# Kernel tuning notes

Measured on AMD Instinct MI355X. Metric: run time of the kernel, lower is better.

Reference implementation:

```python
import math
import jax, jax.numpy as jnp
import numpy as np

SCALE = math.sqrt(128.0)  # NOTE: original code MULTIPLIES by sqrt(128)
DROPOUT_P = 0.1


def setup_inputs() -> dict:
    key = jax.random.key(0)
    kq, kk, kv = jax.random.split(key, 3)
    B, Q, V, H = 4, 4096, 4096, 128
    return {
        "query": jax.random.normal(kq, (B, Q, H), dtype=jnp.float32),
        "key": jax.random.normal(kk, (B, V, H), dtype=jnp.float32),
        "value": jax.random.normal(kv, (B, V, H), dtype=jnp.float32),
    }


def reference(query, key, value):
    # qk: [B, Q, V]
    qk = jnp.einsum("bqh,bvh->bqv", query, key)
    scaled_qk = qk * SCALE
    softmax_qk = jax.nn.softmax(scaled_qk, axis=-1)
    # inverted dropout with a fixed RNG key (deterministic reference)
    dk = jax.random.key(42)
    keep = jax.random.bernoulli(dk, 1.0 - DROPOUT_P, softmax_qk.shape)
    dropout_qk = jnp.where(keep, softmax_qk / (1.0 - DROPOUT_P), 0.0)
    # output: [B, Q, H]
    return jnp.einsum("bqv,bvh->bqh", dropout_qk, value)
```

## Files before the change

kernel.cpp:

```cpp
#include <hip/hip_runtime.h>
#include <stdint.h>

#define NBATCH 4
#define NQ 4096
#define NV 4096
#define HD 128

#define SCL2E ((float)(11.31370849898476 * 1.4426950408889634))

#define KEEP_THRESH 3865470464u
#define EPS_SKIP 1e-6f

#define CHK_K(v,c) ((((v) * 16) + (((c) ^ (v)) & 15)) * 8)
#define CHK_V(h,c) ((((h) * 8)  + (((c) ^ (h)) & 7))  * 8)
#define TILE_USH 24576
#define WS_NEEDED ((size_t)NBATCH * 64 * TILE_USH * 2)

#define PSTR 72
#define VLSTR 142

#define KSTR 144
#define VSTR 76

typedef __attribute__((ext_vector_type(8))) short short8;
typedef __attribute__((ext_vector_type(4))) float floatx4;
typedef unsigned int uint;
typedef unsigned short ushort;
typedef __attribute__((address_space(3))) uint lds_u32;
typedef __attribute__((address_space(1))) const uint glb_u32;

__device__ __forceinline__ ushort bf16rne(float f) {
    uint u = __float_as_uint(f);
    u = (u + 0x7fffu + ((u >> 16) & 1u)) >> 16;
    return (ushort)u;
}
__device__ __forceinline__ float bf2f(ushort h) {
    return __uint_as_float(((uint)h) << 16);
}

template <int CTRL>
__device__ __forceinline__ float dppmov(float x) {
    return __int_as_float(__builtin_amdgcn_update_dpp(
        0, __float_as_int(x), CTRL, 0xF, 0xF, true));
}
__device__ __forceinline__ float row_max16(float x) {
    x = fmaxf(x, dppmov<0xB1>(x));
    x = fmaxf(x, dppmov<0x4E>(x));
    x = fmaxf(x, dppmov<0x141>(x));
    x = fmaxf(x, dppmov<0x140>(x));
    return x;
}
__device__ __forceinline__ float row_sum16(float x) {
    x += dppmov<0xB1>(x);
    x += dppmov<0x4E>(x);
    x += dppmov<0x141>(x);
    x += dppmov<0x140>(x);
    return x;
}

__device__ __forceinline__ uint rotl(uint x, int r) { return (x << r) | (x >> (32 - r)); }

__device__ __forceinline__ uint threefry_bits(uint j) {
    uint x0 = 0u;
    uint x1 = j;
    const uint k0 = 0u, k1 = 42u, k2 = 0u ^ 42u ^ 0x1BD11BDAu;
    x0 += k0; x1 += k1;
#define TFR4(a,b,c,d) \
    x0 += x1; x1 = rotl(x1, a); x1 ^= x0; \
    x0 += x1; x1 = rotl(x1, b); x1 ^= x0; \
    x0 += x1; x1 = rotl(x1, c); x1 ^= x0; \
    x0 += x1; x1 = rotl(x1, d); x1 ^= x0;
    TFR4(13, 15, 26, 6)
    x0 += k1; x1 += k2 + 1u;
    TFR4(17, 29, 16, 24)
    x0 += k2; x1 += k0 + 2u;
    TFR4(13, 15, 26, 6)
    x0 += k0; x1 += k1 + 3u;
    TFR4(17, 29, 16, 24)
    x0 += k1; x1 += k2 + 4u;
    TFR4(13, 15, 26, 6)
    x0 += k2; x1 += k0 + 5u;
#undef TFR4
    return x0 ^ x1;
}

__global__ __launch_bounds__(256)
void prepass(const float* __restrict__ Kg, const float* __restrict__ Vg,
             ushort* __restrict__ W) {
    __shared__ ushort vls[64 * VLSTR];
    const int bb = blockIdx.x >> 6;
    const int t  = blockIdx.x & 63;
    const int v0 = t * 64;
    const size_t kvbase = (size_t)bb * NV * HD;
    ushort* dst = W + ((size_t)bb * 64 + t) * TILE_USH;
    ushort* dkh = dst;
    ushort* dkl = dst + 8192;
    ushort* dvt = dst + 16384;
    const int tid = threadIdx.x;

#pragma unroll
    for (int i = 0; i < 4; ++i) {
        int lc = i * 256 + tid;
        int v = lc >> 4, c = lc & 15;
        const float* src = Kg + kvbase + (size_t)(v0 + v) * HD + c * 8;
        float x[8];
        *(float4*)&x[0] = *(const float4*)src;
        *(float4*)&x[4] = *(const float4*)(src + 4);
        uint H[4], L[4];
#pragma unroll
        for (int k = 0; k < 4; ++k) {
            ushort h0 = bf16rne(x[2 * k]),     h1 = bf16rne(x[2 * k + 1]);
            ushort l0 = bf16rne(x[2 * k] - bf2f(h0));
            ushort l1 = bf16rne(x[2 * k + 1] - bf2f(h1));
            H[k] = (uint)h0 | ((uint)h1 << 16);
            L[k] = (uint)l0 | ((uint)l1 << 16);
        }
        int pos = CHK_K(v, c);
        *(uint4*)&dkh[pos] = *(uint4*)H;
        *(uint4*)&dkl[pos] = *(uint4*)L;
    }

#pragma unroll
    for (int i = 0; i < 8; ++i) {
        int idx = i * 256 + tid;
        int v = idx >> 5, hq = idx & 31;
        float4 a = *(const float4*)(Vg + kvbase + (size_t)(v0 + v) * HD + hq * 4);
        uint w0 = (uint)bf16rne(a.x) | ((uint)bf16rne(a.y) << 16);
        uint w1 = (uint)bf16rne(a.z) | ((uint)bf16rne(a.w) << 16);
        *(uint*)&vls[v * VLSTR + hq * 4]     = w0;
        *(uint*)&vls[v * VLSTR + hq * 4 + 2] = w1;
    }
    __syncthreads();
#pragma unroll
    for (int i = 0; i < 4; ++i) {
        int oc = i * 256 + tid;
        int h = oc >> 3, swz = oc & 7;
        int c2 = (swz ^ h) & 7;
        uint Wd[4];
#pragma unroll
        for (int m = 0; m < 8; m += 2) {
            ushort a  = vls[(c2 * 8 + m) * VLSTR + h];
            ushort b2 = vls[(c2 * 8 + m + 1) * VLSTR + h];
            Wd[m >> 1] = (uint)a | ((uint)b2 << 16);
        }
        *(uint4*)&dvt[oc * 8] = *(uint4*)Wd;
    }
}

__global__ __launch_bounds__(256)
void fa_mfma4(const float* __restrict__ Qg, const ushort* __restrict__ Wk,
              float* __restrict__ Og) {
    __shared__ __align__(16) ushort kbuf[2][16384];
    __shared__ __align__(16) ushort vbuf[3][8192];
    __shared__ ushort pls[4][16 * PSTR];

    const int tid  = threadIdx.x;
    const int wave = tid >> 6;
    const int lane = tid & 63;
    const int r    = lane & 15;
    const int qd   = lane >> 4;
    const int blockRow0 = blockIdx.x * 64;
    const int b = blockRow0 >> 12;
    const int waveRow0 = blockRow0 + wave * 16;
    const ushort* kvw = Wk + (size_t)b * 64 * TILE_USH;

    short8 qfh[4], qfl[4];
    {
        const float* qp = Qg + (size_t)(waveRow0 + r) * HD + qd * 8;
#pragma unroll
        for (int kc = 0; kc < 4; ++kc) {
            float x[8];
            *(float4*)&x[0] = *(const float4*)(qp + kc * 32);
            *(float4*)&x[4] = *(const float4*)(qp + kc * 32 + 4);
#pragma unroll
            for (int j = 0; j < 8; ++j) {
                ushort h = bf16rne(x[j]);
                qfh[kc][j] = (short)h;
                qfl[kc][j] = (short)bf16rne(x[j] - bf2f(h));
            }
        }
    }

    floatx4 oacc[8];
#pragma unroll
    for (int n = 0; n < 8; ++n) oacc[n] = (floatx4){0.f, 0.f, 0.f, 0.f};
    float m2[4] = {-INFINITY, -INFINITY, -INFINITY, -INFINITY};
    float lr[4] = {0.f, 0.f, 0.f, 0.f};

#define STAGE(tt, ks, vs) do { \
        const ushort* _sK = kvw + (size_t)(tt) * TILE_USH; \
        const ushort* _sV = _sK + 16384; \
        _Pragma("unroll") \
        for (int _i = 0; _i < 8; ++_i) \
            __builtin_amdgcn_global_load_lds((glb_u32*)(_sK + (_i * 256 + tid) * 8), \
                (lds_u32*)&kbuf[ks][(_i * 256 + wave * 64) * 8], 16, 0, 0); \
        _Pragma("unroll") \
        for (int _i = 0; _i < 4; ++_i) \
            __builtin_amdgcn_global_load_lds((glb_u32*)(_sV + (_i * 256 + tid) * 8), \
                (lds_u32*)&vbuf[vs][(_i * 256 + wave * 64) * 8], 16, 0, 0); \
    } while (0)

    STAGE(0, 0, 0);
    int vprev = 2, vcur = 0, vnext = 1;
    bool prevNeed = false;

    for (int t = 0; t < 64; ++t) {
        __syncthreads();

        if (t < 63) STAGE(t + 1, (t + 1) & 1, vnext);

        const ushort* KH = kbuf[t & 1];
        const ushort* KL = KH + 8192;
        const int v0 = t * 64;

        floatx4 cf[4];
#pragma unroll
        for (int nb = 0; nb < 4; ++nb) cf[nb] = (floatx4){0.f, 0.f, 0.f, 0.f};
#pragma unroll
        for (int kc = 0; kc < 4; ++kc) {
#pragma unroll
            for (int nb = 0; nb < 4; ++nb) {
                int ch = CHK_K(nb * 16 + r, kc * 4 + qd);
                short8 kh = *(const short8*)&KH[ch];
                short8 kl = *(const short8*)&KL[ch];
                cf[nb] = __builtin_amdgcn_mfma_f32_16x16x32_bf16(qfh[kc], kh, cf[nb], 0, 0, 0);
                cf[nb] = __builtin_amdgcn_mfma_f32_16x16x32_bf16(qfh[kc], kl, cf[nb], 0, 0, 0);
                cf[nb] = __builtin_amdgcn_mfma_f32_16x16x32_bf16(qfl[kc], kh, cf[nb], 0, 0, 0);
            }
        }

        if (prevNeed) {
            const ushort* VTp = vbuf[vprev];
#pragma unroll
            for (int kc2 = 0; kc2 < 2; ++kc2) {
                short8 pa = *(const short8*)&pls[wave][r * PSTR + kc2 * 32 + qd * 8];
#pragma unroll
                for (int n = 0; n < 8; ++n) {
                    short8 vb = *(const short8*)&VTp[CHK_V(n * 16 + r, kc2 * 4 + qd)];
                    oacc[n] = __builtin_amdgcn_mfma_f32_16x16x32_bf16(pa, vb, oacc[n], 0, 0, 0);
                }
            }
        }

        float ts[4][4], p[4][4];
#pragma unroll
        for (int nb = 0; nb < 4; ++nb)
#pragma unroll
            for (int g = 0; g < 4; ++g) ts[nb][g] = cf[nb][g] * SCL2E;

        float tsum[4], alpha[4], lnew[4];
#pragma unroll
        for (int g = 0; g < 4; ++g) {
            float tmx = fmaxf(fmaxf(ts[0][g], ts[1][g]), fmaxf(ts[2][g], ts[3][g]));
            tmx = row_max16(tmx);
            float mn = fmaxf(m2[g], tmx);
            alpha[g] = __builtin_amdgcn_exp2f(m2[g] - mn);
            m2[g] = mn;
        }
#pragma unroll
        for (int g = 0; g < 4; ++g) {
            float s = 0.f;
#pragma unroll
            for (int nb = 0; nb < 4; ++nb) {
                p[nb][g] = __builtin_amdgcn_exp2f(ts[nb][g] - m2[g]);
                s += p[nb][g];
            }
            s = row_sum16(s);
            tsum[g] = s;
            lnew[g] = lr[g] * alpha[g] + s;
            lr[g] = lnew[g];
        }

        bool rowneed = false;
#pragma unroll
        for (int g = 0; g < 4; ++g) rowneed |= (tsum[g] > EPS_SKIP * lnew[g]);
        bool act = __any(rowneed);

        if (act) {
#pragma unroll
            for (int n = 0; n < 8; ++n)
#pragma unroll
                for (int g = 0; g < 4; ++g) oacc[n][g] *= alpha[g];

#pragma unroll
            for (int nb = 0; nb < 4; ++nb) {
#pragma unroll
                for (int g = 0; g < 4; ++g) {
                    if (__any(p[nb][g] > EPS_SKIP * lnew[g])) {
                        uint j = (uint)(waveRow0 + qd * 4 + g) * (uint)NV
                               + (uint)(v0 + nb * 16 + r);
                        if (threefry_bits(j) >= KEEP_THRESH) p[nb][g] = 0.f;
                    }
                    pls[wave][(qd * 4 + g) * PSTR + nb * 16 + r] =
                        (ushort)(__float_as_uint(p[nb][g]) >> 16);
                }
            }
            __asm__ volatile("s_waitcnt lgkmcnt(0)" ::: "memory");
        }
        prevNeed = act;
        vprev = vcur; vcur = vnext; vnext = 3 - vprev - vcur;
    }
#undef STAGE

    if (prevNeed) {
        const ushort* VTp = vbuf[vprev];
#pragma unroll
        for (int kc2 = 0; kc2 < 2; ++kc2) {
            short8 pa = *(const short8*)&pls[wave][r * PSTR + kc2 * 32 + qd * 8];
#pragma unroll
            for (int n = 0; n < 8; ++n) {
                short8 vb = *(const short8*)&VTp[CHK_V(n * 16 + r, kc2 * 4 + qd)];
                oacc[n] = __builtin_amdgcn_mfma_f32_16x16x32_bf16(pa, vb, oacc[n], 0, 0, 0);
            }
        }
    }

    float inv[4];
#pragma unroll
    for (int g = 0; g < 4; ++g) inv[g] = 1.0f / (0.9f * lr[g]);
#pragma unroll
    for (int n = 0; n < 8; ++n)
#pragma unroll
        for (int g = 0; g < 4; ++g)
            Og[(size_t)(waveRow0 + qd * 4 + g) * HD + n * 16 + r] = oacc[n][g] * inv[g];
}

__global__ __launch_bounds__(256)
void fa_mfma(const float* __restrict__ Qg, const float* __restrict__ Kg,
             const float* __restrict__ Vg, float* __restrict__ Og) {
    __shared__ ushort khi[64 * KSTR];
    __shared__ ushort klo[64 * KSTR];
    __shared__ ushort vt[128 * VSTR];
    __shared__ ushort plsf[4][16 * PSTR];

    const int tid  = threadIdx.x;
    const int wave = tid >> 6;
    const int lane = tid & 63;
    const int r    = lane & 15;
    const int qd   = lane >> 4;
    const int blockRow0 = blockIdx.x * 64;
    const int b = blockRow0 >> 12;
    const int waveRow0 = blockRow0 + wave * 16;
    const size_t kvbase = (size_t)b * NV * HD;

    short8 qfh[4], qfl[4];
    {
        const float* qp = Qg + (size_t)(waveRow0 + r) * HD + qd * 8;
#pragma unroll
        for (int kc = 0; kc < 4; ++kc) {
            float x[8];
            *(float4*)&x[0] = *(const float4*)(qp + kc * 32);
            *(float4*)&x[4] = *(const float4*)(qp + kc * 32 + 4);
#pragma unroll
            for (int j = 0; j < 8; ++j) {
                ushort h = bf16rne(x[j]);
                qfh[kc][j] = (short)h;
                qfl[kc][j] = (short)bf16rne(x[j] - bf2f(h));
            }
        }
    }

    floatx4 oacc[8];
#pragma unroll
    for (int n = 0; n < 8; ++n) oacc[n] = (floatx4){0.f, 0.f, 0.f, 0.f};
    float m2[4] = {-INFINITY, -INFINITY, -INFINITY, -INFINITY};
    float lr[4] = {0.f, 0.f, 0.f, 0.f};

    for (int v0 = 0; v0 < NV; v0 += 64) {
        __syncthreads();
#pragma unroll
        for (int i = 0; i < 8; ++i) {
            int f = i * 256 + tid;
            int v = f >> 5;
            int h = (f & 31) * 4;
            float4 kv = *(const float4*)(Kg + kvbase + (size_t)(v0 + v) * HD + h);
            ushort4 hh, ll;
            hh.x = bf16rne(kv.x); ll.x = bf16rne(kv.x - bf2f(hh.x));
            hh.y = bf16rne(kv.y); ll.y = bf16rne(kv.y - bf2f(hh.y));
            hh.z = bf16rne(kv.z); ll.z = bf16rne(kv.z - bf2f(hh.z));
            hh.w = bf16rne(kv.w); ll.w = bf16rne(kv.w - bf2f(hh.w));
            *(ushort4*)&khi[v * KSTR + h] = hh;
            *(ushort4*)&klo[v * KSTR + h] = ll;
        }
        {
            int hp = tid & 63, rp = tid >> 6;
            int h = hp * 2;
            const float* vpb = Vg + kvbase + (size_t)v0 * HD + h;
#pragma unroll
            for (int i = 0; i < 8; ++i) {
                int v = i * 8 + rp * 2;
                float2 a = *(const float2*)(vpb + (size_t)v * HD);
                float2 c = *(const float2*)(vpb + (size_t)(v + 1) * HD);
                uint w0 = (uint)bf16rne(a.x) | ((uint)bf16rne(c.x) << 16);
                uint w1 = (uint)bf16rne(a.y) | ((uint)bf16rne(c.y) << 16);
                *(uint*)&vt[h * VSTR + v]       = w0;
                *(uint*)&vt[(h + 1) * VSTR + v] = w1;
            }
        }
        __syncthreads();

        floatx4 cf[4];
#pragma unroll
        for (int nb = 0; nb < 4; ++nb) cf[nb] = (floatx4){0.f, 0.f, 0.f, 0.f};
#pragma unroll
        for (int kc = 0; kc < 4; ++kc) {
#pragma unroll
            for (int nb = 0; nb < 4; ++nb) {
                int off = (nb * 16 + r) * KSTR + kc * 32 + qd * 8;
                short8 kh = *(const short8*)&khi[off];
                short8 kl = *(const short8*)&klo[off];
                cf[nb] = __builtin_amdgcn_mfma_f32_16x16x32_bf16(qfh[kc], kh, cf[nb], 0, 0, 0);
                cf[nb] = __builtin_amdgcn_mfma_f32_16x16x32_bf16(qfh[kc], kl, cf[nb], 0, 0, 0);
                cf[nb] = __builtin_amdgcn_mfma_f32_16x16x32_bf16(qfl[kc], kh, cf[nb], 0, 0, 0);
            }
        }

        float ts[4][4], p[4][4];
#pragma unroll
        for (int nb = 0; nb < 4; ++nb)
#pragma unroll
            for (int g = 0; g < 4; ++g) ts[nb][g] = cf[nb][g] * SCL2E;

        float tsum[4], alpha[4], lnew[4];
#pragma unroll
        for (int g = 0; g < 4; ++g) {
            float tmx = fmaxf(fmaxf(ts[0][g], ts[1][g]), fmaxf(ts[2][g], ts[3][g]));
#pragma unroll
            for (int off = 1; off < 16; off <<= 1)
                tmx = fmaxf(tmx, __shfl_xor(tmx, off));
            float mn = fmaxf(m2[g], tmx);
            alpha[g] = __builtin_amdgcn_exp2f(m2[g] - mn);
            m2[g] = mn;
        }
#pragma unroll
        for (int g = 0; g < 4; ++g) {
            float s = 0.f;
#pragma unroll
            for (int nb = 0; nb < 4; ++nb) {
                p[nb][g] = __builtin_amdgcn_exp2f(ts[nb][g] - m2[g]);
                s += p[nb][g];
            }
#pragma unroll
            for (int off = 1; off < 16; off <<= 1)
                s += __shfl_xor(s, off);
            tsum[g] = s;
            lnew[g] = lr[g] * alpha[g] + s;
            lr[g] = lnew[g];
        }

        bool rowneed = false;
#pragma unroll
        for (int g = 0; g < 4; ++g) rowneed |= (tsum[g] > 1e-8f * lnew[g]);

        if (__any(rowneed)) {
#pragma unroll
            for (int n = 0; n < 8; ++n)
#pragma unroll
                for (int g = 0; g < 4; ++g) oacc[n][g] *= alpha[g];

#pragma unroll
            for (int nb = 0; nb < 4; ++nb) {
                bool nbneed = false;
#pragma unroll
                for (int g = 0; g < 4; ++g) nbneed |= (p[nb][g] > 1e-8f * lnew[g]);
                if (__any(nbneed)) {
#pragma unroll
                    for (int g = 0; g < 4; ++g) {
                        uint j = (uint)(waveRow0 + qd * 4 + g) * (uint)NV
                               + (uint)(v0 + nb * 16 + r);
                        if (threefry_bits(j) >= KEEP_THRESH) p[nb][g] = 0.f;
                    }
                }
#pragma unroll
                for (int g = 0; g < 4; ++g)
                    plsf[wave][(qd * 4 + g) * PSTR + nb * 16 + r] = bf16rne(p[nb][g]);
            }
            __asm__ volatile("s_waitcnt lgkmcnt(0)" ::: "memory");

#pragma unroll
            for (int kc2 = 0; kc2 < 2; ++kc2) {
                short8 pa = *(const short8*)&plsf[wave][r * PSTR + kc2 * 32 + qd * 8];
#pragma unroll
                for (int n = 0; n < 8; ++n) {
                    int off = (n * 16 + r) * VSTR + kc2 * 32 + qd * 8;
                    ushort4 u0 = *(const ushort4*)&vt[off];
                    ushort4 u1 = *(const ushort4*)&vt[off + 4];
                    short8 vb;
                    vb[0] = (short)u0.x; vb[1] = (short)u0.y; vb[2] = (short)u0.z; vb[3] = (short)u0.w;
                    vb[4] = (short)u1.x; vb[5] = (short)u1.y; vb[6] = (short)u1.z; vb[7] = (short)u1.w;
                    oacc[n] = __builtin_amdgcn_mfma_f32_16x16x32_bf16(pa, vb, oacc[n], 0, 0, 0);
                }
            }
        }
    }

    float inv[4];
#pragma unroll
    for (int g = 0; g < 4; ++g) inv[g] = 1.0f / (0.9f * lr[g]);
#pragma unroll
    for (int n = 0; n < 8; ++n)
#pragma unroll
        for (int g = 0; g < 4; ++g)
            Og[(size_t)(waveRow0 + qd * 4 + g) * HD + n * 16 + r] = oacc[n][g] * inv[g];
}

extern "C" void kernel_launch(void* const* d_in, const int* in_sizes, int n_in,
                              void* d_out, int out_size, void* d_ws, size_t ws_size,
                              hipStream_t stream) {
    (void)in_sizes; (void)n_in; (void)out_size;
    const float* Qg = (const float*)d_in[0];
    const float* Kg = (const float*)d_in[1];
    const float* Vg = (const float*)d_in[2];
    float* Og = (float*)d_out;
    if (ws_size >= WS_NEEDED) {
        prepass<<<dim3(256), 256, 0, stream>>>(Kg, Vg, (ushort*)d_ws);
        fa_mfma4<<<dim3(NBATCH * NQ / 64), 256, 0, stream>>>(Qg, (const ushort*)d_ws, Og);
    } else {
        fa_mfma<<<dim3(NBATCH * NQ / 64), 256, 0, stream>>>(Qg, Kg, Vg, Og);
    }
}
```

Before: 236.6 us.

## Split KV tiles across wave pairs and read fragments directly from global memory

The attention kernel now gives each 16-row group two waves that process alternating KV tiles. The two partial softmax states and accumulators are merged through shared memory at the end. K and V fragments are loaded straight from global memory in an MFMA-fragment-ordered layout that the prepass now writes, replacing the LDS staging and barriers. The prepass is split into separate K and V halves. This removes per-tile block synchronisation and LDS traffic and doubles the grid, at the cost of relying on cache for K/V reuse and adding a final merge step.

```diff
diff --git a/kernel.cpp b/kernel.cpp
--- a/kernel.cpp
+++ b/kernel.cpp
@@ -11,8 +11,6 @@
 #define KEEP_THRESH 3865470464u
 #define EPS_SKIP 1e-6f
 
-#define CHK_K(v,c) ((((v) * 16) + (((c) ^ (v)) & 15)) * 8)
-#define CHK_V(h,c) ((((h) * 8)  + (((c) ^ (h)) & 7))  * 8)
 #define TILE_USH 24576
 #define WS_NEEDED ((size_t)NBATCH * 64 * TILE_USH * 2)
 
@@ -26,8 +24,6 @@
 typedef __attribute__((ext_vector_type(4))) float floatx4;
 typedef unsigned int uint;
 typedef unsigned short ushort;
-typedef __attribute__((address_space(3))) uint lds_u32;
-typedef __attribute__((address_space(1))) const uint glb_u32;
 
 __device__ __forceinline__ ushort bf16rne(float f) {
     uint u = __float_as_uint(f);
@@ -88,80 +84,86 @@
 void prepass(const float* __restrict__ Kg, const float* __restrict__ Vg,
              ushort* __restrict__ W) {
     __shared__ ushort vls[64 * VLSTR];
-    const int bb = blockIdx.x >> 6;
-    const int t  = blockIdx.x & 63;
+    const int rec  = blockIdx.x >> 1;
+    const int half = blockIdx.x & 1;
+    const int bb = rec >> 6;
+    const int t  = rec & 63;
     const int v0 = t * 64;
     const size_t kvbase = (size_t)bb * NV * HD;
     ushort* dst = W + ((size_t)bb * 64 + t) * TILE_USH;
-    ushort* dkh = dst;
-    ushort* dkl = dst + 8192;
-    ushort* dvt = dst + 16384;
     const int tid = threadIdx.x;
 
-#pragma unroll
-    for (int i = 0; i < 4; ++i) {
-        int lc = i * 256 + tid;
-        int v = lc >> 4, c = lc & 15;
-        const float* src = Kg + kvbase + (size_t)(v0 + v) * HD + c * 8;
-        float x[8];
-        *(float4*)&x[0] = *(const float4*)src;
-        *(float4*)&x[4] = *(const float4*)(src + 4);
-        uint H[4], L[4];
-#pragma unroll
-        for (int k = 0; k < 4; ++k) {
-            ushort h0 = bf16rne(x[2 * k]),     h1 = bf16rne(x[2 * k + 1]);
-            ushort l0 = bf16rne(x[2 * k] - bf2f(h0));
-            ushort l1 = bf16rne(x[2 * k + 1] - bf2f(h1));
-            H[k] = (uint)h0 | ((uint)h1 << 16);
-            L[k] = (uint)l0 | ((uint)l1 << 16);
-        }
-        int pos = CHK_K(v, c);
-        *(uint4*)&dkh[pos] = *(uint4*)H;
-        *(uint4*)&dkl[pos] = *(uint4*)L;
-    }
-
-#pragma unroll
-    for (int i = 0; i < 8; ++i) {
-        int idx = i * 256 + tid;
-        int v = idx >> 5, hq = idx & 31;
-        float4 a = *(const float4*)(Vg + kvbase + (size_t)(v0 + v) * HD + hq * 4);
-        uint w0 = (uint)bf16rne(a.x) | ((uint)bf16rne(a.y) << 16);
-        uint w1 = (uint)bf16rne(a.z) | ((uint)bf16rne(a.w) << 16);
-        *(uint*)&vls[v * VLSTR + hq * 4]     = w0;
-        *(uint*)&vls[v * VLSTR + hq * 4 + 2] = w1;
-    }
-    __syncthreads();
-#pragma unroll
-    for (int i = 0; i < 4; ++i) {
-        int oc = i * 256 + tid;
-        int h = oc >> 3, swz = oc & 7;
-        int c2 = (swz ^ h) & 7;
-        uint Wd[4];
-#pragma unroll
-        for (int m = 0; m < 8; m += 2) {
-            ushort a  = vls[(c2 * 8 + m) * VLSTR + h];
-            ushort b2 = vls[(c2 * 8 + m + 1) * VLSTR + h];
-            Wd[m >> 1] = (uint)a | ((uint)b2 << 16);
-        }
-        *(uint4*)&dvt[oc * 8] = *(uint4*)Wd;
-    }
-}
-
-__global__ __launch_bounds__(256)
-void fa_mfma4(const float* __restrict__ Qg, const ushort* __restrict__ Wk,
+    if (half == 0) {
+        ushort* dkh = dst;
+        ushort* dkl = dst + 8192;
+#pragma unroll
+        for (int i = 0; i < 4; ++i) {
+            int lc = i * 256 + tid;
+            int v = lc >> 4, c = lc & 15;
+            const float* src = Kg + kvbase + (size_t)(v0 + v) * HD + c * 8;
+            float x[8];
+            *(float4*)&x[0] = *(const float4*)src;
+            *(float4*)&x[4] = *(const float4*)(src + 4);
+            uint H[4], L[4];
+#pragma unroll
+            for (int k = 0; k < 4; ++k) {
+                ushort h0 = bf16rne(x[2 * k]),     h1 = bf16rne(x[2 * k + 1]);
+                ushort l0 = bf16rne(x[2 * k] - bf2f(h0));
+                ushort l1 = bf16rne(x[2 * k + 1] - bf2f(h1));
+                H[k] = (uint)h0 | ((uint)h1 << 16);
+                L[k] = (uint)l0 | ((uint)l1 << 16);
+            }
+            int pos = (((c >> 2) * 4 + (v >> 4)) * 64 + (c & 3) * 16 + (v & 15)) * 8;
+            *(uint4*)&dkh[pos] = *(uint4*)H;
+            *(uint4*)&dkl[pos] = *(uint4*)L;
+        }
+    } else {
+        ushort* dvt = dst + 16384;
+#pragma unroll
+        for (int i = 0; i < 8; ++i) {
+            int idx = i * 256 + tid;
+            int v = idx >> 5, hq = idx & 31;
+            float4 a = *(const float4*)(Vg + kvbase + (size_t)(v0 + v) * HD + hq * 4);
+            uint w0 = (uint)bf16rne(a.x) | ((uint)bf16rne(a.y) << 16);
+            uint w1 = (uint)bf16rne(a.z) | ((uint)bf16rne(a.w) << 16);
+            *(uint*)&vls[v * VLSTR + hq * 4]     = w0;
+            *(uint*)&vls[v * VLSTR + hq * 4 + 2] = w1;
+        }
+        __syncthreads();
+#pragma unroll
+        for (int i = 0; i < 4; ++i) {
+            int lc = i * 256 + tid;
+            int h = lc >> 3, c2 = lc & 7;
+            uint Wd[4];
+#pragma unroll
+            for (int m = 0; m < 8; m += 2) {
+                ushort a  = vls[(c2 * 8 + m) * VLSTR + h];
+                ushort b2 = vls[(c2 * 8 + m + 1) * VLSTR + h];
+                Wd[m >> 1] = (uint)a | ((uint)b2 << 16);
+            }
+            int pos = (((c2 >> 2) * 8 + (h >> 4)) * 64 + (c2 & 3) * 16 + (h & 15)) * 8;
+            *(uint4*)&dvt[pos] = *(uint4*)Wd;
+        }
+    }
+}
+
+__global__ __launch_bounds__(256, 2)
+void fa_mfma6(const float* __restrict__ Qg, const ushort* __restrict__ Wk,
               float* __restrict__ Og) {
-    __shared__ __align__(16) ushort kbuf[2][16384];
-    __shared__ __align__(16) ushort vbuf[3][8192];
     __shared__ ushort pls[4][16 * PSTR];
+    __shared__ float mbuf[2][16 * 128];
+    __shared__ float mlbuf[2][16][2];
 
     const int tid  = threadIdx.x;
     const int wave = tid >> 6;
     const int lane = tid & 63;
     const int r    = lane & 15;
     const int qd   = lane >> 4;
-    const int blockRow0 = blockIdx.x * 64;
+    const int rg   = wave >> 1;
+    const int th   = wave & 1;
+    const int blockRow0 = blockIdx.x * 32;
     const int b = blockRow0 >> 12;
-    const int waveRow0 = blockRow0 + wave * 16;
+    const int waveRow0 = blockRow0 + rg * 16;
     const ushort* kvw = Wk + (size_t)b * 64 * TILE_USH;
 
     short8 qfh[4], qfl[4];
@@ -187,30 +189,9 @@
     float m2[4] = {-INFINITY, -INFINITY, -INFINITY, -INFINITY};
     float lr[4] = {0.f, 0.f, 0.f, 0.f};
 
-#define STAGE(tt, ks, vs) do { \
-        const ushort* _sK = kvw + (size_t)(tt) * TILE_USH; \
-        const ushort* _sV = _sK + 16384; \
-        _Pragma("unroll") \
-        for (int _i = 0; _i < 8; ++_i) \
-            __builtin_amdgcn_global_load_lds((glb_u32*)(_sK + (_i * 256 + tid) * 8), \
-                (lds_u32*)&kbuf[ks][(_i * 256 + wave * 64) * 8], 16, 0, 0); \
-        _Pragma("unroll") \
-        for (int _i = 0; _i < 4; ++_i) \
-            __builtin_amdgcn_global_load_lds((glb_u32*)(_sV + (_i * 256 + tid) * 8), \
-                (lds_u32*)&vbuf[vs][(_i * 256 + wave * 64) * 8], 16, 0, 0); \
-    } while (0)
-
-    STAGE(0, 0, 0);
-    int vprev = 2, vcur = 0, vnext = 1;
-    bool prevNeed = false;
-
-    for (int t = 0; t < 64; ++t) {
-        __syncthreads();
-
-        if (t < 63) STAGE(t + 1, (t + 1) & 1, vnext);
-
-        const ushort* KH = kbuf[t & 1];
-        const ushort* KL = KH + 8192;
+    for (int t = th; t < 64; t += 2) {
+        const ushort* tK = kvw + (size_t)t * TILE_USH;
+        const ushort* tV = tK + 16384;
         const int v0 = t * 64;
 
         floatx4 cf[4];
@@ -218,27 +199,18 @@
         for (int nb = 0; nb < 4; ++nb) cf[nb] = (floatx4){0.f, 0.f, 0.f, 0.f};
 #pragma unroll
         for (int kc = 0; kc < 4; ++kc) {
-#pragma unroll
-            for (int nb = 0; nb < 4; ++nb) {
-                int ch = CHK_K(nb * 16 + r, kc * 4 + qd);
-                short8 kh = *(const short8*)&KH[ch];
-                short8 kl = *(const short8*)&KL[ch];
-                cf[nb] = __builtin_amdgcn_mfma_f32_16x16x32_bf16(qfh[kc], kh, cf[nb], 0, 0, 0);
-                cf[nb] = __builtin_amdgcn_mfma_f32_16x16x32_bf16(qfh[kc], kl, cf[nb], 0, 0, 0);
-                cf[nb] = __builtin_amdgcn_mfma_f32_16x16x32_bf16(qfl[kc], kh, cf[nb], 0, 0, 0);
-            }
-        }
-
-        if (prevNeed) {
-            const ushort* VTp = vbuf[vprev];
-#pragma unroll
-            for (int kc2 = 0; kc2 < 2; ++kc2) {
-                short8 pa = *(const short8*)&pls[wave][r * PSTR + kc2 * 32 + qd * 8];
-#pragma unroll
-                for (int n = 0; n < 8; ++n) {
-                    short8 vb = *(const short8*)&VTp[CHK_V(n * 16 + r, kc2 * 4 + qd)];
-                    oacc[n] = __builtin_amdgcn_mfma_f32_16x16x32_bf16(pa, vb, oacc[n], 0, 0, 0);
-                }
+            short8 kh[4], kl[4];
+#pragma unroll
+            for (int nb = 0; nb < 4; ++nb) {
+                int off = ((kc * 4 + nb) * 64 + lane) * 8;
+                kh[nb] = *(const short8*)&tK[off];
+                kl[nb] = *(const short8*)&tK[8192 + off];
+            }
+#pragma unroll
+            for (int nb = 0; nb < 4; ++nb) {
+                cf[nb] = __builtin_amdgcn_mfma_f32_16x16x32_bf16(qfh[kc], kh[nb], cf[nb], 0, 0, 0);
+                cf[nb] = __builtin_amdgcn_mfma_f32_16x16x32_bf16(qfh[kc], kl[nb], cf[nb], 0, 0, 0);
+                cf[nb] = __builtin_amdgcn_mfma_f32_16x16x32_bf16(qfl[kc], kh[nb], cf[nb], 0, 0, 0);
             }
         }
 
@@ -274,9 +246,8 @@
         bool rowneed = false;
 #pragma unroll
         for (int g = 0; g < 4; ++g) rowneed |= (tsum[g] > EPS_SKIP * lnew[g]);
-        bool act = __any(rowneed);
-
-        if (act) {
+
+        if (__any(rowneed)) {
 #pragma unroll
             for (int n = 0; n < 8; ++n)
 #pragma unroll
@@ -296,33 +267,55 @@
                 }
             }
             __asm__ volatile("s_waitcnt lgkmcnt(0)" ::: "memory");
-        }
-        prevNeed = act;
-        vprev = vcur; vcur = vnext; vnext = 3 - vprev - vcur;
-    }
-#undef STAGE
-
-    if (prevNeed) {
-        const ushort* VTp = vbuf[vprev];
-#pragma unroll
-        for (int kc2 = 0; kc2 < 2; ++kc2) {
-            short8 pa = *(const short8*)&pls[wave][r * PSTR + kc2 * 32 + qd * 8];
-#pragma unroll
-            for (int n = 0; n < 8; ++n) {
-                short8 vb = *(const short8*)&VTp[CHK_V(n * 16 + r, kc2 * 4 + qd)];
-                oacc[n] = __builtin_amdgcn_mfma_f32_16x16x32_bf16(pa, vb, oacc[n], 0, 0, 0);
-            }
-        }
-    }
-
-    float inv[4];
-#pragma unroll
-    for (int g = 0; g < 4; ++g) inv[g] = 1.0f / (0.9f * lr[g]);
-#pragma unroll
-    for (int n = 0; n < 8; ++n)
-#pragma unroll
-        for (int g = 0; g < 4; ++g)
-            Og[(size_t)(waveRow0 + qd * 4 + g) * HD + n * 16 + r] = oacc[n][g] * inv[g];
+
+#pragma unroll
+            for (int kc2 = 0; kc2 < 2; ++kc2) {
+                short8 pa = *(const short8*)&pls[wave][r * PSTR + kc2 * 32 + qd * 8];
+#pragma unroll
+                for (int n = 0; n < 8; ++n) {
+                    short8 vb = *(const short8*)&tV[((kc2 * 8 + n) * 64 + lane) * 8];
+                    oacc[n] = __builtin_amdgcn_mfma_f32_16x16x32_bf16(pa, vb, oacc[n], 0, 0, 0);
+                }
+            }
+        }
+    }
+
+    if (th == 1) {
+        if (r == 0) {
+#pragma unroll
+            for (int g = 0; g < 4; ++g) {
+                mlbuf[rg][qd * 4 + g][0] = m2[g];
+                mlbuf[rg][qd * 4 + g][1] = lr[g];
+            }
+        }
+#pragma unroll
+        for (int n = 0; n < 8; ++n)
+#pragma unroll
+            for (int g = 0; g < 4; ++g)
+                mbuf[rg][(qd * 4 + g) * 128 + n * 16 + r] = oacc[n][g];
+    }
+    __syncthreads();
+    if (th == 0) {
+        float aA[4], aB[4], inv[4];
+#pragma unroll
+        for (int g = 0; g < 4; ++g) {
+            float mo = mlbuf[rg][qd * 4 + g][0];
+            float so = mlbuf[rg][qd * 4 + g][1];
+            float mn = fmaxf(m2[g], mo);
+            aA[g] = __builtin_amdgcn_exp2f(m2[g] - mn);
+            aB[g] = __builtin_amdgcn_exp2f(mo - mn);
+            float l = lr[g] * aA[g] + so * aB[g];
+            inv[g] = 1.0f / (0.9f * l);
+        }
+#pragma unroll
+        for (int n = 0; n < 8; ++n)
+#pragma unroll
+            for (int g = 0; g < 4; ++g) {
+                float o = oacc[n][g] * aA[g]
+                        + mbuf[rg][(qd * 4 + g) * 128 + n * 16 + r] * aB[g];
+                Og[(size_t)(waveRow0 + qd * 4 + g) * HD + n * 16 + r] = o * inv[g];
+            }
+    }
 }
 
 __global__ __launch_bounds__(256)
@@ -513,8 +506,9 @@
     const float* Vg = (const float*)d_in[2];
     float* Og = (float*)d_out;
     if (ws_size >= WS_NEEDED) {
-        prepass<<<dim3(256), 256, 0, stream>>>(Kg, Vg, (ushort*)d_ws);
-        fa_mfma4<<<dim3(NBATCH * NQ / 64), 256, 0, stream>>>(Qg, (const ushort*)d_ws, Og);
+        ushort* W = (ushort*)d_ws;
+        prepass<<<dim3(512), 256, 0, stream>>>(Kg, Vg, W);
+        fa_mfma6<<<dim3(NBATCH * NQ / 32), 256, 0, stream>>>(Qg, (const ushort*)W, Og);
     } else {
         fa_mfma<<<dim3(NBATCH * NQ / 64), 256, 0, stream>>>(Qg, Kg, Vg, Og);
     }
```

Result: slower. 247.2 us (+4.5%).
